# Kernel tuning notes

Measured on AMD Instinct MI355X. Metric: run time of the kernel, lower is better.

## Reference

```python
import jax, jax.numpy as jnp
import numpy as np

B, S, P, L, H = 64, 512, 32, 30, 768
FH = 1024  # fc_hidden_size


def setup_inputs() -> dict:
    key = jax.random.key(0)
    ks = jax.random.split(key, 8)
    token_embeddings = jax.random.normal(ks[0], (B, S, H), jnp.float32)
    pooler_output = jax.random.normal(ks[1], (B, H), jnp.float32)
    num_positions = jax.random.randint(ks[2], (B, P), 0, S)
    # labels: 0/1 codes, with trailing slots per example padded with -1 rows
    lab = jax.random.randint(ks[3], (B, P, L), 0, 2).astype(jnp.float32)
    valid = jax.random.randint(ks[4], (B, 1), 8, P + 1)  # num real slots per example
    row = jnp.arange(P)[None, :]
    lab = jnp.where((row < valid)[:, :, None], lab, -1.0)
    num_codes_labels = lab.reshape(B, P * L)
    W1 = jax.random.normal(ks[5], (2 * H, FH), jnp.float32) / np.sqrt(2 * H)
    b1 = jnp.zeros((FH,), jnp.float32)
    W2 = jax.random.normal(ks[6], (FH, FH // 2), jnp.float32) / np.sqrt(FH)
    b2 = jnp.zeros((FH // 2,), jnp.float32)
    W3 = jax.random.normal(ks[7], (FH // 2, L), jnp.float32) / np.sqrt(FH // 2)
    b3 = jnp.zeros((L,), jnp.float32)
    return {"token_embeddings": token_embeddings, "pooler_output": pooler_output,
            "num_positions": num_positions, "num_codes_labels": num_codes_labels,
            "W1": W1, "b1": b1, "W2": W2, "b2": b2, "W3": W3, "b3": b3}


def reference(token_embeddings, pooler_output, num_positions, num_codes_labels,
              W1, b1, W2, b2, W3, b3):
    # gather number-token hidden states: [B, P, H]
    p_hidden = jnp.take_along_axis(token_embeddings, num_positions[:, :, None], axis=1)
    feat = jnp.concatenate(
        [p_hidden, jnp.broadcast_to(pooler_output[:, None, :], p_hidden.shape)], axis=-1)
    # Batch_Net_CLS head. NOTE: original uses nn.LeakyReLU(True) -> negative_slope=1.0,
    # which is mathematically the identity, so the activations are omitted (faithful).
    h = feat @ W1 + b1
    h = h @ W2 + b2
    logits = h @ W3 + b3  # [B, P, L]

    labels = num_codes_labels.reshape(B, -1, L)
    pad_pre = jnp.any(labels != -1.0, axis=-1)  # [B, P] True for real slots
    mf = pad_pre.astype(jnp.float32)

    # BCEWithLogitsLoss over non-pad elements: softplus(x) - x*y, mean
    bce_elem = jax.nn.softplus(logits) - logits * labels
    bce_loss = jnp.sum(bce_elem * mf[:, :, None]) / (jnp.sum(mf) * L)

    binary = (jax.nn.sigmoid(logits) > 0.5).astype(jnp.float32)
    count_out = jnp.sum(binary, axis=-1)
    count_lab = jnp.sum(labels, axis=-1)
    count_loss = jnp.mean((count_out - count_lab) ** 2 * mf)

    # position loss: only slots where both counts are exactly 1 (single-hot)
    eq = (count_out == 1.0) & (count_lab == 1.0)
    pos_out = jnp.argmax(binary, axis=-1).astype(jnp.float32)
    pos_lab = jnp.argmax(labels, axis=-1).astype(jnp.float32)
    n_eq = jnp.sum(eq.astype(jnp.float32))
    pos_sum = jnp.sum((pos_out - pos_lab) ** 2 * eq.astype(jnp.float32))
    position_loss = jnp.where(n_eq > 0, pos_sum / jnp.maximum(n_eq, 1.0), 0.0)

    return bce_loss + 10.0 * count_loss + 5.0 * position_loss
```

## Files before the change

### kernel.cpp

```cpp
#include <hip/hip_runtime.h>
#include <cstddef>
#include <cstdint>

#define Mq   2048
#define Lq   30
#define N1q  1024
#define N2q  512
#define K1q  1536
#define Hq   768
#define NBLK 512

typedef float    f32x4 __attribute__((ext_vector_type(4)));
typedef _Float16 f16x8 __attribute__((ext_vector_type(8)));

#define GLD16(gptr, lptr) \
  __builtin_amdgcn_global_load_lds((const __attribute__((address_space(1))) void*)(gptr), \
                                   (__attribute__((address_space(3))) void*)(lptr), 16, 0, 0)

__device__ void transpose_tile(const float* __restrict__ src,
                               _Float16* __restrict__ dst,
                               int K, int N, int k0, int n0) {
  __shared__ float T[64][65];
  const int t = threadIdx.x;
  {
    const int kl = t >> 2, nc = (t & 3) * 16;
    const float* s = src + (size_t)(k0 + kl) * N + n0 + nc;
    float4 v0 = *(const float4*)s;
    float4 v1 = *(const float4*)(s + 4);
    float4 v2 = *(const float4*)(s + 8);
    float4 v3 = *(const float4*)(s + 12);
    T[nc + 0][kl] = v0.x; T[nc + 1][kl] = v0.y; T[nc + 2][kl] = v0.z; T[nc + 3][kl] = v0.w;
    T[nc + 4][kl] = v1.x; T[nc + 5][kl] = v1.y; T[nc + 6][kl] = v1.z; T[nc + 7][kl] = v1.w;
    T[nc + 8][kl] = v2.x; T[nc + 9][kl] = v2.y; T[nc +10][kl] = v2.z; T[nc +11][kl] = v2.w;
    T[nc +12][kl] = v3.x; T[nc +13][kl] = v3.y; T[nc +14][kl] = v3.z; T[nc +15][kl] = v3.w;
  }
  __syncthreads();
  {
    const int nl = t >> 2, kc = (t & 3) * 16;
    __align__(16) _Float16 tmp[16];
    #pragma unroll
    for (int i = 0; i < 16; ++i) tmp[i] = (_Float16)T[nl][kc + i];
    _Float16* d = dst + (size_t)(n0 + nl) * K + k0 + kc;
    *(uint4*)d       = *(const uint4*)tmp;
    *(uint4*)(d + 8) = *(const uint4*)(tmp + 8);
  }
}

__global__ __launch_bounds__(256)
void prep_all(const float* __restrict__ tok, const float* __restrict__ pool,
              const int* __restrict__ npos, const float* __restrict__ W1,
              const float* __restrict__ W2, const float* __restrict__ W3,
              const float* __restrict__ b2, const float* __restrict__ b3,
              _Float16* __restrict__ A1, _Float16* __restrict__ W1T,
              float* __restrict__ W23T, float* __restrict__ beff) {
  const int bid = blockIdx.x, tid = threadIdx.x;
  if (bid < 256) {
    const int q = tid >> 5, l32 = tid & 31;
    const int m = bid * 8 + q;
    const int bI = m >> 5, p = m & 31;
    const int pos = npos[bI * 32 + p];
    const float* src1 = tok + ((size_t)bI * 512 + pos) * Hq;
    const float* src2 = pool + (size_t)bI * Hq;
    _Float16* dst = A1 + (size_t)m * K1q;
    for (int g = l32; g < 384; g += 32) {
      const float* s = (g < 192) ? (src1 + g * 4) : (src2 + (g - 192) * 4);
      float4 v = *(const float4*)s;
      __align__(8) _Float16 o[4] = {(_Float16)v.x, (_Float16)v.y, (_Float16)v.z, (_Float16)v.w};
      *(uint2*)(dst + g * 4) = *(const uint2*)o;
    }
  } else if (bid < 640) {
    const int idx = bid - 256;
    transpose_tile(W1, W1T, K1q, N1q, (idx / 16) * 64, (idx % 16) * 64);
  } else if (bid < 760) {
    const int idx = (bid - 640) * 256 + tid;
    const int k = idx / Lq, c = idx - k * Lq;
    const float* w2r = W2 + (size_t)k * N2q;
    float s0 = 0.f, s1 = 0.f, s2 = 0.f, s3 = 0.f;
    #pragma unroll 4
    for (int j = 0; j < N2q; j += 4) {
      const float4 wv = *(const float4*)(w2r + j);
      s0 = fmaf(wv.x, W3[(size_t)(j)     * Lq + c], s0);
      s1 = fmaf(wv.y, W3[(size_t)(j + 1) * Lq + c], s1);
      s2 = fmaf(wv.z, W3[(size_t)(j + 2) * Lq + c], s2);
      s3 = fmaf(wv.w, W3[(size_t)(j + 3) * Lq + c], s3);
    }
    W23T[(size_t)c * N1q + k] = (s0 + s1) + (s2 + s3);
  } else {
    __shared__ float R[8][32];
    const int c = tid % Lq, jc = tid / Lq;
    float s = 0.f;
    if (tid < 240) {
      for (int j = jc * 64; j < jc * 64 + 64; ++j)
        s = fmaf(b2[j], W3[(size_t)j * Lq + c], s);
      R[jc][c] = s;
    }
    __syncthreads();
    if (tid < Lq) {
      float t0 = b3[tid];
      #pragma unroll
      for (int g = 0; g < 8; ++g) t0 += R[g][tid];
      beff[tid] = t0;
    }
  }
}

__global__ __launch_bounds__(256)
void gemm1_k(const _Float16* __restrict__ A, const _Float16* __restrict__ BT,
             const float* __restrict__ b1, _Float16* __restrict__ C1) {
  __shared__ _Float16 As[2][64 * 64];
  __shared__ _Float16 Bs[2][64 * 64];
  const int tid = threadIdx.x, w = tid >> 6, lane = tid & 63;
  const int n0 = blockIdx.x * 64, m0 = blockIdx.y * 64;
  const int ml = lane & 15, g4 = lane >> 4;
  const int wm = (w >> 1) * 32, wn = (w & 1) * 32;
  const int lr = lane >> 3, lc = lane & 7;

  f32x4 acc[2][2];
  #pragma unroll
  for (int i = 0; i < 2; ++i)
    #pragma unroll
    for (int j = 0; j < 2; ++j)
      #pragma unroll
      for (int r = 0; r < 4; ++r) acc[i][j][r] = 0.f;

  auto stage = [&](int it, int b) {
    const int kt = it * 64;
    #pragma unroll
    for (int t = 0; t < 2; ++t) {
      const int r  = w * 16 + t * 8 + lr;
      const int cs = lc ^ (r & 7);
      GLD16(A  + (size_t)(m0 + r) * K1q + kt + cs * 8, &As[b][(w * 16 + t * 8) * 64]);
      GLD16(BT + (size_t)(n0 + r) * K1q + kt + cs * 8, &Bs[b][(w * 16 + t * 8) * 64]);
    }
  };

  stage(0, 0);
  __syncthreads();
  #pragma unroll 1
  for (int it = 0; it < 24; ++it) {
    const int cur = it & 1;
    if (it < 23) stage(it + 1, cur ^ 1);
    f16x8 af[2][2], bf[2][2];
    #pragma unroll
    for (int i = 0; i < 2; ++i) {
      const int ar = wm + i * 16 + ml;
      const int br = wn + i * 16 + ml;
      #pragma unroll
      for (int ks = 0; ks < 2; ++ks) {
        af[i][ks] = *(const f16x8*)&As[cur][ar * 64 + (((ks * 4 + g4) ^ (ar & 7)) << 3)];
        bf[i][ks] = *(const f16x8*)&Bs[cur][br * 64 + (((ks * 4 + g4) ^ (br & 7)) << 3)];
      }
    }
    #pragma unroll
    for (int i = 0; i < 2; ++i)
      #pragma unroll
      for (int j = 0; j < 2; ++j)
        #pragma unroll
        for (int ks = 0; ks < 2; ++ks)
          acc[i][j] = __builtin_amdgcn_mfma_f32_16x16x32_f16(bf[j][ks], af[i][ks], acc[i][j], 0, 0, 0);
    __syncthreads();
  }

  #pragma unroll
  for (int i = 0; i < 2; ++i) {
    const int row = m0 + wm + i * 16 + ml;
    #pragma unroll
    for (int j = 0; j < 2; ++j) {
      const int col = n0 + wn + j * 16 + g4 * 4;
      const float4 bv = *(const float4*)(b1 + col);
      __align__(8) _Float16 o[4] = {(_Float16)(acc[i][j][0] + bv.x),
                                    (_Float16)(acc[i][j][1] + bv.y),
                                    (_Float16)(acc[i][j][2] + bv.z),
                                    (_Float16)(acc[i][j][3] + bv.w)};
      *(uint2*)(C1 + (size_t)row * N1q + col) = *(const uint2*)o;
    }
  }
}

__global__ __launch_bounds__(256)
void loss_kernel(const _Float16* __restrict__ C1, const float* __restrict__ W23T,
                 const float* __restrict__ beff, const float* __restrict__ labels,
                 float* __restrict__ part) {
  __shared__ float hrow[4][1024];
  __shared__ float red[4][5];
  const int tid = threadIdx.x, w = tid >> 6, lane = tid & 63;
  const int m = blockIdx.x * 4 + w;

  {
    const int k = lane * 16;
    const _Float16* cp = C1 + (size_t)m * N1q + k;
    f16x8 v0 = *(const f16x8*)cp;
    f16x8 v1 = *(const f16x8*)(cp + 8);
    #pragma unroll
    for (int e = 0; e < 8; ++e) {
      hrow[w][k + e]     = (float)v0[e];
      hrow[w][k + 8 + e] = (float)v1[e];
    }
  }
  __syncthreads();

  const int c  = lane & 31;
  const int kh = lane >> 5;
  float a0 = 0.f, a1 = 0.f, a2 = 0.f, a3 = 0.f;
  if (c < Lq) {
    const float* hp = hrow[w] + kh * 512;
    const float* wp = W23T + (size_t)c * N1q + kh * 512;
    #pragma unroll 4
    for (int i = 0; i < 512; i += 4) {
      const float4 wv = *(const float4*)(wp + i);
      a0 = fmaf(hp[i],     wv.x, a0);
      a1 = fmaf(hp[i + 1], wv.y, a1);
      a2 = fmaf(hp[i + 2], wv.z, a2);
      a3 = fmaf(hp[i + 3], wv.w, a3);
    }
  }
  float a = (a0 + a1) + (a2 + a3);
  a += __shfl_xor(a, 32);

  const bool act = lane < Lq;
  float logit = 0.f, lab = 0.f;
  if (act) {
    logit = a + beff[lane];
    lab = labels[(size_t)m * Lq + lane];
  }

  const unsigned long long validmask = __ballot(act && lab != -1.0f);
  const unsigned long long outmask   = __ballot(act && logit > 0.0f);
  const unsigned long long labmask   = __ballot(act && lab == 1.0f);
  const bool valid = (validmask != 0ULL);
  const int count_out = __popcll(outmask);
  const int count_lab = __popcll(labmask);

  float bce = 0.f;
  if (act && valid) {
    const float x = logit;
    bce = fmaxf(x, 0.f) + log1pf(expf(-fabsf(x))) - x * lab;
  }
  bce += __shfl_xor(bce, 16); bce += __shfl_xor(bce, 8);
  bce += __shfl_xor(bce, 4);  bce += __shfl_xor(bce, 2);
  bce += __shfl_xor(bce, 1);

  if (lane == 0) {
    float pb = 0.f, pv = 0.f, pc = 0.f, pe = 0.f, pp = 0.f;
    if (valid) {
      pb = bce; pv = 1.f;
      const float d = (float)count_out - (float)count_lab;
      pc = d * d;
    }
    if (count_out == 1 && count_lab == 1) {
      const float po = (float)(__ffsll((long long)outmask) - 1);
      const float pl = (float)(__ffsll((long long)labmask) - 1);
      pe = 1.f;
      const float dp = po - pl;
      pp = dp * dp;
    }
    red[w][0] = pb; red[w][1] = pv; red[w][2] = pc; red[w][3] = pe; red[w][4] = pp;
  }
  __syncthreads();
  if (tid < 5) {
    part[blockIdx.x * 5 + tid] =
        red[0][tid] + red[1][tid] + red[2][tid] + red[3][tid];
  }
}

__global__ __launch_bounds__(256)
void finalize_kernel(const float* __restrict__ part, float* __restrict__ out) {
  __shared__ float red[32][5];
  const int t = threadIdx.x;
  if (t < 160) {
    const int j = t % 5, grp = t / 5;
    float s = 0.f;
    for (int i = grp; i < NBLK; i += 32) s += part[i * 5 + j];
    red[grp][j] = s;
  }
  __syncthreads();
  if (t == 0) {
    float t0 = 0.f, t1 = 0.f, t2 = 0.f, t3 = 0.f, t4 = 0.f;
    #pragma unroll
    for (int g = 0; g < 32; ++g) {
      t0 += red[g][0]; t1 += red[g][1]; t2 += red[g][2];
      t3 += red[g][3]; t4 += red[g][4];
    }
    const float bce = t0 / (t1 * (float)Lq);
    const float cnt = 10.0f * t2 / (float)Mq;
    const float pos = (t3 > 0.f) ? 5.0f * t4 / fmaxf(t3, 1.0f) : 0.f;
    out[0] = bce + cnt + pos;
  }
}

extern "C" void kernel_launch(void* const* d_in, const int* in_sizes, int n_in,
                              void* d_out, int out_size, void* d_ws, size_t ws_size,
                              hipStream_t stream) {
  const float* tok    = (const float*)d_in[0];
  const float* pool   = (const float*)d_in[1];
  const int*   npos   = (const int*)  d_in[2];
  const float* labels = (const float*)d_in[3];
  const float* W1     = (const float*)d_in[4];
  const float* b1     = (const float*)d_in[5];
  const float* W2     = (const float*)d_in[6];
  const float* b2     = (const float*)d_in[7];
  const float* W3     = (const float*)d_in[8];
  const float* b3     = (const float*)d_in[9];
  float* out = (float*)d_out;

  char* ws = (char*)d_ws;
  _Float16* A1   = (_Float16*)(ws + 0x00000000);
  _Float16* W1T  = (_Float16*)(ws + 0x00600000);
  _Float16* C1   = (_Float16*)(ws + 0x00900000);
  float*    W23T = (float*)   (ws + 0x00D00000);
  float*    beff = (float*)   (ws + 0x00D20000);
  float*    part = (float*)   (ws + 0x00D30000);

  prep_all<<<761, 256, 0, stream>>>(tok, pool, npos, W1, W2, W3, b2, b3,
                                    A1, W1T, W23T, beff);
  gemm1_k<<<dim3(16, 32), 256, 0, stream>>>(A1, W1T, b1, C1);
  loss_kernel<<<NBLK, 256, 0, stream>>>(C1, W23T, beff, labels, part);
  finalize_kernel<<<1, 256, 0, stream>>>(part, out);
}
```

Baseline: 213.3 us.

## Collapse all three linear layers into one 1536x30 weight and skip GEMM

Because the activations are identity, W1·W2·W3 is precomputed into a single 1536x30 fp32 matrix, with a combined bias, in two small prep kernels. The loss kernel then gathers token and pooler rows straight into shared memory and computes the logits from the folded weight. This removes the fp16 conversion of activations, the W1 transpose, and the 2048x1024x1536 MFMA GEMM along with its intermediate buffer. In exchange there are two dependent prep launches, and the per-row dot products in the loss kernel now read the weight with a stride of 30 floats.

```diff
diff --git a/kernel.cpp b/kernel.cpp
--- a/kernel.cpp
+++ b/kernel.cpp
@@ -10,191 +10,117 @@
 #define Hq   768
 #define NBLK 512
 
-typedef float    f32x4 __attribute__((ext_vector_type(4)));
-typedef _Float16 f16x8 __attribute__((ext_vector_type(8)));
-
-#define GLD16(gptr, lptr) \
-  __builtin_amdgcn_global_load_lds((const __attribute__((address_space(1))) void*)(gptr), \
-                                   (__attribute__((address_space(3))) void*)(lptr), 16, 0, 0)
-
-__device__ void transpose_tile(const float* __restrict__ src,
-                               _Float16* __restrict__ dst,
-                               int K, int N, int k0, int n0) {
-  __shared__ float T[64][65];
-  const int t = threadIdx.x;
+
+__global__ __launch_bounds__(256)
+void prep1(const float* __restrict__ W2, const float* __restrict__ W3,
+           const float* __restrict__ b2, const float* __restrict__ b3,
+           float* __restrict__ W23, float* __restrict__ beff23) {
+  const int bid = blockIdx.x, tid = threadIdx.x;
+  if (bid < 120) {
+    __shared__ float Ws[7680];
+    const int idx = bid * 256 + tid;
+    const int k = idx / Lq, c = idx - k * Lq;
+    const float* w2r = W2 + (size_t)k * N2q;
+    float s0 = 0.f, s1 = 0.f, s2 = 0.f, s3 = 0.f;
+    for (int half = 0; half < 2; ++half) {
+      __syncthreads();
+      for (int i = tid * 4; i < 7680; i += 1024)
+        *(float4*)&Ws[i] = *(const float4*)&W3[half * 7680 + i];
+      __syncthreads();
+      const float* w2h = w2r + half * 256;
+      #pragma unroll 4
+      for (int j = 0; j < 256; j += 4) {
+        const float4 wv = *(const float4*)(w2h + j);
+        s0 = fmaf(wv.x, Ws[(j    ) * Lq + c], s0);
+        s1 = fmaf(wv.y, Ws[(j + 1) * Lq + c], s1);
+        s2 = fmaf(wv.z, Ws[(j + 2) * Lq + c], s2);
+        s3 = fmaf(wv.w, Ws[(j + 3) * Lq + c], s3);
+      }
+    }
+    W23[idx] = (s0 + s1) + (s2 + s3);
+  } else {
+    __shared__ float R[8][32];
+    const int c = tid % Lq, jc = tid / Lq;
+    if (tid < 240) {
+      float s = 0.f;
+      for (int j = jc * 64; j < jc * 64 + 64; ++j)
+        s = fmaf(b2[j], W3[(size_t)j * Lq + c], s);
+      R[jc][c] = s;
+    }
+    __syncthreads();
+    if (tid < Lq) {
+      float t = b3[tid];
+      #pragma unroll
+      for (int g = 0; g < 8; ++g) t += R[g][tid];
+      beff23[tid] = t;
+    }
+  }
+}
+
+__global__ __launch_bounds__(256)
+void prep2(const float* __restrict__ W1, const float* __restrict__ b1,
+           const float* __restrict__ W23, const float* __restrict__ beff23,
+           float* __restrict__ W123, float* __restrict__ btot) {
+  const int bid = blockIdx.x, tid = threadIdx.x;
+  if (bid < 180) {
+    __shared__ float Ws[7680];
+    const int idx = bid * 256 + tid;
+    const int k = idx / Lq, c = idx - k * Lq;
+    const float* w1r = W1 + (size_t)k * N1q;
+    float s0 = 0.f, s1 = 0.f, s2 = 0.f, s3 = 0.f;
+    for (int ph = 0; ph < 4; ++ph) {
+      __syncthreads();
+      for (int i = tid * 4; i < 7680; i += 1024)
+        *(float4*)&Ws[i] = *(const float4*)&W23[ph * 7680 + i];
+      __syncthreads();
+      const float* w1h = w1r + ph * 256;
+      #pragma unroll 4
+      for (int j = 0; j < 256; j += 4) {
+        const float4 wv = *(const float4*)(w1h + j);
+        s0 = fmaf(wv.x, Ws[(j    ) * Lq + c], s0);
+        s1 = fmaf(wv.y, Ws[(j + 1) * Lq + c], s1);
+        s2 = fmaf(wv.z, Ws[(j + 2) * Lq + c], s2);
+        s3 = fmaf(wv.w, Ws[(j + 3) * Lq + c], s3);
+      }
+    }
+    W123[idx] = (s0 + s1) + (s2 + s3);
+  } else {
+    __shared__ float R[8][32];
+    const int c = tid % Lq, jc = tid / Lq;
+    if (tid < 240) {
+      float s = 0.f;
+      for (int j = jc * 128; j < jc * 128 + 128; ++j)
+        s = fmaf(b1[j], W23[(size_t)j * Lq + c], s);
+      R[jc][c] = s;
+    }
+    __syncthreads();
+    if (tid < Lq) {
+      float t = beff23[tid];
+      #pragma unroll
+      for (int g = 0; g < 8; ++g) t += R[g][tid];
+      btot[tid] = t;
+    }
+  }
+}
+
+__global__ __launch_bounds__(256)
+void loss_kernel(const float* __restrict__ tok, const float* __restrict__ pool,
+                 const int* __restrict__ npos, const float* __restrict__ W123,
+                 const float* __restrict__ btot, const float* __restrict__ labels,
+                 float* __restrict__ part) {
+  __shared__ float hrow[4][1536];
+  __shared__ float red[4][5];
+  const int tid = threadIdx.x, w = tid >> 6, lane = tid & 63;
+  const int m = blockIdx.x * 4 + w;
+  const int bI = m >> 5, p = m & 31;
+
   {
-    const int kl = t >> 2, nc = (t & 3) * 16;
-    const float* s = src + (size_t)(k0 + kl) * N + n0 + nc;
-    float4 v0 = *(const float4*)s;
-    float4 v1 = *(const float4*)(s + 4);
-    float4 v2 = *(const float4*)(s + 8);
-    float4 v3 = *(const float4*)(s + 12);
-    T[nc + 0][kl] = v0.x; T[nc + 1][kl] = v0.y; T[nc + 2][kl] = v0.z; T[nc + 3][kl] = v0.w;
-    T[nc + 4][kl] = v1.x; T[nc + 5][kl] = v1.y; T[nc + 6][kl] = v1.z; T[nc + 7][kl] = v1.w;
-    T[nc + 8][kl] = v2.x; T[nc + 9][kl] = v2.y; T[nc +10][kl] = v2.z; T[nc +11][kl] = v2.w;
-    T[nc +12][kl] = v3.x; T[nc +13][kl] = v3.y; T[nc +14][kl] = v3.z; T[nc +15][kl] = v3.w;
-  }
-  __syncthreads();
-  {
-    const int nl = t >> 2, kc = (t & 3) * 16;
-    __align__(16) _Float16 tmp[16];
-    #pragma unroll
-    for (int i = 0; i < 16; ++i) tmp[i] = (_Float16)T[nl][kc + i];
-    _Float16* d = dst + (size_t)(n0 + nl) * K + k0 + kc;
-    *(uint4*)d       = *(const uint4*)tmp;
-    *(uint4*)(d + 8) = *(const uint4*)(tmp + 8);
-  }
-}
-
-__global__ __launch_bounds__(256)
-void prep_all(const float* __restrict__ tok, const float* __restrict__ pool,
-              const int* __restrict__ npos, const float* __restrict__ W1,
-              const float* __restrict__ W2, const float* __restrict__ W3,
-              const float* __restrict__ b2, const float* __restrict__ b3,
-              _Float16* __restrict__ A1, _Float16* __restrict__ W1T,
-              float* __restrict__ W23T, float* __restrict__ beff) {
-  const int bid = blockIdx.x, tid = threadIdx.x;
-  if (bid < 256) {
-    const int q = tid >> 5, l32 = tid & 31;
-    const int m = bid * 8 + q;
-    const int bI = m >> 5, p = m & 31;
     const int pos = npos[bI * 32 + p];
     const float* src1 = tok + ((size_t)bI * 512 + pos) * Hq;
     const float* src2 = pool + (size_t)bI * Hq;
-    _Float16* dst = A1 + (size_t)m * K1q;
-    for (int g = l32; g < 384; g += 32) {
+    for (int g = lane; g < 384; g += 64) {
       const float* s = (g < 192) ? (src1 + g * 4) : (src2 + (g - 192) * 4);
-      float4 v = *(const float4*)s;
-      __align__(8) _Float16 o[4] = {(_Float16)v.x, (_Float16)v.y, (_Float16)v.z, (_Float16)v.w};
-      *(uint2*)(dst + g * 4) = *(const uint2*)o;
-    }
-  } else if (bid < 640) {
-    const int idx = bid - 256;
-    transpose_tile(W1, W1T, K1q, N1q, (idx / 16) * 64, (idx % 16) * 64);
-  } else if (bid < 760) {
-    const int idx = (bid - 640) * 256 + tid;
-    const int k = idx / Lq, c = idx - k * Lq;
-    const float* w2r = W2 + (size_t)k * N2q;
-    float s0 = 0.f, s1 = 0.f, s2 = 0.f, s3 = 0.f;
-    #pragma unroll 4
-    for (int j = 0; j < N2q; j += 4) {
-      const float4 wv = *(const float4*)(w2r + j);
-      s0 = fmaf(wv.x, W3[(size_t)(j)     * Lq + c], s0);
-      s1 = fmaf(wv.y, W3[(size_t)(j + 1) * Lq + c], s1);
-      s2 = fmaf(wv.z, W3[(size_t)(j + 2) * Lq + c], s2);
-      s3 = fmaf(wv.w, W3[(size_t)(j + 3) * Lq + c], s3);
-    }
-    W23T[(size_t)c * N1q + k] = (s0 + s1) + (s2 + s3);
-  } else {
-    __shared__ float R[8][32];
-    const int c = tid % Lq, jc = tid / Lq;
-    float s = 0.f;
-    if (tid < 240) {
-      for (int j = jc * 64; j < jc * 64 + 64; ++j)
-        s = fmaf(b2[j], W3[(size_t)j * Lq + c], s);
-      R[jc][c] = s;
-    }
-    __syncthreads();
-    if (tid < Lq) {
-      float t0 = b3[tid];
-      #pragma unroll
-      for (int g = 0; g < 8; ++g) t0 += R[g][tid];
-      beff[tid] = t0;
-    }
-  }
-}
-
-__global__ __launch_bounds__(256)
-void gemm1_k(const _Float16* __restrict__ A, const _Float16* __restrict__ BT,
-             const float* __restrict__ b1, _Float16* __restrict__ C1) {
-  __shared__ _Float16 As[2][64 * 64];
-  __shared__ _Float16 Bs[2][64 * 64];
-  const int tid = threadIdx.x, w = tid >> 6, lane = tid & 63;
-  const int n0 = blockIdx.x * 64, m0 = blockIdx.y * 64;
-  const int ml = lane & 15, g4 = lane >> 4;
-  const int wm = (w >> 1) * 32, wn = (w & 1) * 32;
-  const int lr = lane >> 3, lc = lane & 7;
-
-  f32x4 acc[2][2];
-  #pragma unroll
-  for (int i = 0; i < 2; ++i)
-    #pragma unroll
-    for (int j = 0; j < 2; ++j)
-      #pragma unroll
-      for (int r = 0; r < 4; ++r) acc[i][j][r] = 0.f;
-
-  auto stage = [&](int it, int b) {
-    const int kt = it * 64;
-    #pragma unroll
-    for (int t = 0; t < 2; ++t) {
-      const int r  = w * 16 + t * 8 + lr;
-      const int cs = lc ^ (r & 7);
-      GLD16(A  + (size_t)(m0 + r) * K1q + kt + cs * 8, &As[b][(w * 16 + t * 8) * 64]);
-      GLD16(BT + (size_t)(n0 + r) * K1q + kt + cs * 8, &Bs[b][(w * 16 + t * 8) * 64]);
-    }
-  };
-
-  stage(0, 0);
-  __syncthreads();
-  #pragma unroll 1
-  for (int it = 0; it < 24; ++it) {
-    const int cur = it & 1;
-    if (it < 23) stage(it + 1, cur ^ 1);
-    f16x8 af[2][2], bf[2][2];
-    #pragma unroll
-    for (int i = 0; i < 2; ++i) {
-      const int ar = wm + i * 16 + ml;
-      const int br = wn + i * 16 + ml;
-      #pragma unroll
-      for (int ks = 0; ks < 2; ++ks) {
-        af[i][ks] = *(const f16x8*)&As[cur][ar * 64 + (((ks * 4 + g4) ^ (ar & 7)) << 3)];
-        bf[i][ks] = *(const f16x8*)&Bs[cur][br * 64 + (((ks * 4 + g4) ^ (br & 7)) << 3)];
-      }
-    }
-    #pragma unroll
-    for (int i = 0; i < 2; ++i)
-      #pragma unroll
-      for (int j = 0; j < 2; ++j)
-        #pragma unroll
-        for (int ks = 0; ks < 2; ++ks)
-          acc[i][j] = __builtin_amdgcn_mfma_f32_16x16x32_f16(bf[j][ks], af[i][ks], acc[i][j], 0, 0, 0);
-    __syncthreads();
-  }
-
-  #pragma unroll
-  for (int i = 0; i < 2; ++i) {
-    const int row = m0 + wm + i * 16 + ml;
-    #pragma unroll
-    for (int j = 0; j < 2; ++j) {
-      const int col = n0 + wn + j * 16 + g4 * 4;
-      const float4 bv = *(const float4*)(b1 + col);
-      __align__(8) _Float16 o[4] = {(_Float16)(acc[i][j][0] + bv.x),
-                                    (_Float16)(acc[i][j][1] + bv.y),
-                                    (_Float16)(acc[i][j][2] + bv.z),
-                                    (_Float16)(acc[i][j][3] + bv.w)};
-      *(uint2*)(C1 + (size_t)row * N1q + col) = *(const uint2*)o;
-    }
-  }
-}
-
-__global__ __launch_bounds__(256)
-void loss_kernel(const _Float16* __restrict__ C1, const float* __restrict__ W23T,
-                 const float* __restrict__ beff, const float* __restrict__ labels,
-                 float* __restrict__ part) {
-  __shared__ float hrow[4][1024];
-  __shared__ float red[4][5];
-  const int tid = threadIdx.x, w = tid >> 6, lane = tid & 63;
-  const int m = blockIdx.x * 4 + w;
-
-  {
-    const int k = lane * 16;
-    const _Float16* cp = C1 + (size_t)m * N1q + k;
-    f16x8 v0 = *(const f16x8*)cp;
-    f16x8 v1 = *(const f16x8*)(cp + 8);
-    #pragma unroll
-    for (int e = 0; e < 8; ++e) {
-      hrow[w][k + e]     = (float)v0[e];
-      hrow[w][k + 8 + e] = (float)v1[e];
+      *(float4*)&hrow[w][g * 4] = *(const float4*)s;
     }
   }
   __syncthreads();
@@ -203,15 +129,14 @@
   const int kh = lane >> 5;
   float a0 = 0.f, a1 = 0.f, a2 = 0.f, a3 = 0.f;
   if (c < Lq) {
-    const float* hp = hrow[w] + kh * 512;
-    const float* wp = W23T + (size_t)c * N1q + kh * 512;
+    const float* hp = hrow[w] + kh * 768;
+    const float* wp = W123 + (size_t)(kh * 768) * Lq + c;
     #pragma unroll 4
-    for (int i = 0; i < 512; i += 4) {
-      const float4 wv = *(const float4*)(wp + i);
-      a0 = fmaf(hp[i],     wv.x, a0);
-      a1 = fmaf(hp[i + 1], wv.y, a1);
-      a2 = fmaf(hp[i + 2], wv.z, a2);
-      a3 = fmaf(hp[i + 3], wv.w, a3);
+    for (int i = 0; i < 768; i += 4) {
+      a0 = fmaf(hp[i],     wp[(i)     * Lq], a0);
+      a1 = fmaf(hp[i + 1], wp[(i + 1) * Lq], a1);
+      a2 = fmaf(hp[i + 2], wp[(i + 2) * Lq], a2);
+      a3 = fmaf(hp[i + 3], wp[(i + 3) * Lq], a3);
     }
   }
   float a = (a0 + a1) + (a2 + a3);
@@ -220,7 +145,7 @@
   const bool act = lane < Lq;
   float logit = 0.f, lab = 0.f;
   if (act) {
-    logit = a + beff[lane];
+    logit = a + btot[lane];
     lab = labels[(size_t)m * Lq + lane];
   }
 
@@ -304,16 +229,14 @@
   float* out = (float*)d_out;
 
   char* ws = (char*)d_ws;
-  _Float16* A1   = (_Float16*)(ws + 0x00000000);
-  _Float16* W1T  = (_Float16*)(ws + 0x00600000);
-  _Float16* C1   = (_Float16*)(ws + 0x00900000);
-  float*    W23T = (float*)   (ws + 0x00D00000);
-  float*    beff = (float*)   (ws + 0x00D20000);
-  float*    part = (float*)   (ws + 0x00D30000);
-
-  prep_all<<<761, 256, 0, stream>>>(tok, pool, npos, W1, W2, W3, b2, b3,
-                                    A1, W1T, W23T, beff);
-  gemm1_k<<<dim3(16, 32), 256, 0, stream>>>(A1, W1T, b1, C1);
-  loss_kernel<<<NBLK, 256, 0, stream>>>(C1, W23T, beff, labels, part);
+  float* W23    = (float*)(ws + 0x00000000);
+  float* W123   = (float*)(ws + 0x00020000);
+  float* beff23 = (float*)(ws + 0x00050000);
+  float* btot   = (float*)(ws + 0x00050200);
+  float* part   = (float*)(ws + 0x00051000);
+
+  prep1<<<121, 256, 0, stream>>>(W2, W3, b2, b3, W23, beff23);
+  prep2<<<181, 256, 0, stream>>>(W1, b1, W23, beff23, W123, btot);
+  loss_kernel<<<NBLK, 256, 0, stream>>>(tok, pool, npos, W123, btot, labels, part);
   finalize_kernel<<<1, 256, 0, stream>>>(part, out);
 }
```

New measurement: 207.6 us. 1.03x faster.
